# Kernel tuning notes

Measured on AMD Instinct MI355X. Metric: run time of the kernel, lower is better.

## Reference

```python
import jax, jax.numpy as jnp
import numpy as np
from jax import lax

EPS = 1e-6

def _pixel_coords(loc, H, W):
    # normalized [-1,1] xy -> continuous pixel coordinates (x in [.. W-0.5], y likewise)
    wh = jnp.array([W, H], dtype=loc.dtype)
    pos = 0.5 * (jnp.clip(loc, -1.0, 1.0) + 1.0) * wh - 0.5
    return pos[..., 0], pos[..., 1]

def token2map_agg_sparse(x, loc_orig, idx_agg, H, W):
    # scatter token features to the [H,W] map via nearest pixel of each original point,
    # normalized by per-pixel hit count (sparse-matrix formulation in the original).
    B, N, C = x.shape
    N0 = idx_agg.shape[1]
    px, py = _pixel_coords(loc_orig, H, W)
    ix = jnp.clip(jnp.round(px).astype(jnp.int32), 0, W - 1)
    iy = jnp.clip(jnp.round(py).astype(jnp.int32), 0, H - 1)
    idx_hw = (iy * W + ix + jnp.arange(B, dtype=jnp.int32)[:, None] * (H * W)).reshape(-1)
    vals = jnp.take_along_axis(x, idx_agg[..., None].astype(jnp.int32), axis=1)  # [B,N0,C]
    num = jax.ops.segment_sum(vals.reshape(B * N0, C), idx_hw, num_segments=B * H * W)
    cnt = jax.ops.segment_sum(jnp.ones((B * N0,), x.dtype), idx_hw, num_segments=B * H * W)
    fmap = num / (cnt + EPS)[:, None]
    return fmap.reshape(B, H, W, C).transpose(0, 3, 1, 2)  # NCHW

def map2token_agg_mat(fmap, loc_orig, idx_agg, agg_weight, N):
    # bilinear gather at each original point, then weighted aggregation to tokens via idx_agg
    B, C, H, W = fmap.shape
    N0 = idx_agg.shape[1]
    px, py = _pixel_coords(loc_orig, H, W)
    x0 = jnp.clip(jnp.floor(px).astype(jnp.int32), 0, W - 1)
    x1 = jnp.clip(x0 + 1, 0, W - 1)
    y0 = jnp.clip(jnp.floor(py).astype(jnp.int32), 0, H - 1)
    y1 = jnp.clip(y0 + 1, 0, H - 1)
    wx = jnp.minimum(x1.astype(px.dtype), px) - x0.astype(px.dtype)
    wy = jnp.minimum(y1.astype(py.dtype), py) - y0.astype(py.dtype)
    fm = fmap.transpose(0, 2, 3, 1).reshape(B, H * W, C)
    def gather(iy, ix):
        return jnp.take_along_axis(fm, (iy * W + ix)[..., None], axis=1)
    f = ((1 - wx) * (1 - wy))[..., None] * gather(y0, x0) \
      + (wx * (1 - wy))[..., None] * gather(y0, x1) \
      + ((1 - wx) * wy)[..., None] * gather(y1, x0) \
      + (wx * wy)[..., None] * gather(y1, x1)  # [B,N0,C]
    seg = (idx_agg.astype(jnp.int32) + jnp.arange(B, dtype=jnp.int32)[:, None] * N).reshape(-1)
    w = agg_weight.reshape(B * N0)
    wsum = jax.ops.segment_sum(w, seg, num_segments=B * N) + EPS
    wn = w / wsum[seg]
    out = jax.ops.segment_sum(f.reshape(B * N0, C) * wn[:, None], seg, num_segments=B * N)
    return out.reshape(B, N, C)

def dwconv2d(xmap, conv_w, conv_b):
    C = xmap.shape[1]
    y = lax.conv_general_dilated(xmap, conv_w, (1, 1), ((1, 1), (1, 1)),
                                 feature_group_count=C,
                                 dimension_numbers=('NCHW', 'OIHW', 'NCHW'))
    return y + conv_b[None, :, None, None]

def setup_inputs() -> dict:
    key = jax.random.key(0)
    ks = jax.random.split(key, 6)
    B, N, C, N0, H, W = 16, 1536, 768, 3072, 64, 48
    x = jax.random.normal(ks[0], (B, N, C), dtype=jnp.float32)
    loc = jax.random.uniform(ks[1], (B, N, 2), dtype=jnp.float32) * 2.0 - 1.0
    loc_orig = jax.random.uniform(ks[2], (B, N0, 2), dtype=jnp.float32) * 2.0 - 1.0
    idx_agg = jax.random.randint(ks[3], (B, N0), 0, N, dtype=jnp.int32)
    agg_weight = jax.random.uniform(ks[4], (B, N0, 1), dtype=jnp.float32)
    conv_w = jax.random.normal(ks[5], (C, 1, 3, 3), dtype=jnp.float32) * 0.1
    conv_b = jnp.zeros((C,), dtype=jnp.float32)
    return {"x": x, "loc": loc, "loc_orig": loc_orig, "idx_agg": idx_agg,
            "agg_weight": agg_weight, "H": H, "W": W,
            "conv_w": conv_w, "conv_b": conv_b}

def reference(x, loc, loc_orig, idx_agg, agg_weight, H, W, conv_w, conv_b):
    B, N, C = x.shape
    fmap = token2map_agg_sparse(x, loc_orig, idx_agg, H, W)       # [B,C,H,W]
    fmap = dwconv2d(fmap, conv_w, conv_b)                          # depthwise 3x3
    out = map2token_agg_mat(fmap, loc_orig, idx_agg, agg_weight, N)  # [B,N,C]
    return out
```

## Files before the change

kernel.cpp:

```cpp
#include <hip/hip_runtime.h>

#define B_    16
#define N_    1536
#define C_    768
#define N0_   3072
#define H_    64
#define W_    48
#define HW_   (H_ * W_)
#define NPTS  (B_ * N0_)
#define NTOK  (B_ * N_)
#define NPIX  (B_ * HW_)
#define NSCAN (NPIX + NTOK)
#define NBP   (NPIX / 256)
#define NBALL (NSCAN / 256)
#define EPS_  1e-6f
#define TY_   4
#define TX_   8
#define NTILE ((W_ / TX_) * (H_ / TY_))
#define NBCV  (B_ * NTILE)

__device__ __forceinline__ int xcd_swz(int bid, int n) {
    return (bid & 7) * (n >> 3) + (bid >> 3);
}

__global__ void k_wT(const float* __restrict__ w, float* __restrict__ wT) {
    int i = blockIdx.x * blockDim.x + threadIdx.x;
    if (i < C_ * 9) { int c = i / 9, k = i - c * 9; wT[k * C_ + c] = w[i]; }
}

__global__ void k_points(const float* __restrict__ loc_orig,
                         const int* __restrict__ idx_agg,
                         const float* __restrict__ agg_w,
                         int* __restrict__ pixkey, int4* __restrict__ ofs4,
                         float* __restrict__ wxa, float* __restrict__ wya,
                         float* __restrict__ wa,
                         int* __restrict__ cnt_pix, int* __restrict__ cnt_tok,
                         float* __restrict__ wsum) {
    int i = blockIdx.x * blockDim.x + threadIdx.x;
    if (i >= NPTS) return;
    int b = i / N0_;
    float lx = loc_orig[2 * (size_t)i];
    float ly = loc_orig[2 * (size_t)i + 1];
    lx = fminf(fmaxf(lx, -1.f), 1.f);
    ly = fminf(fmaxf(ly, -1.f), 1.f);
    float px = 0.5f * (lx + 1.f) * (float)W_ - 0.5f;
    float py = 0.5f * (ly + 1.f) * (float)H_ - 0.5f;
    int ixn = min(max((int)rintf(px), 0), W_ - 1);
    int iyn = min(max((int)rintf(py), 0), H_ - 1);
    int pk = b * HW_ + iyn * W_ + ixn;
    pixkey[i] = pk;
    int x0 = min(max((int)floorf(px), 0), W_ - 1);
    int x1 = min(x0 + 1, W_ - 1);
    int y0 = min(max((int)floorf(py), 0), H_ - 1);
    int y1 = min(y0 + 1, H_ - 1);
    wxa[i] = fminf((float)x1, px) - (float)x0;
    wya[i] = fminf((float)y1, py) - (float)y0;
    ofs4[i] = make_int4(y0 * W_ + x0, y0 * W_ + x1, y1 * W_ + x0, y1 * W_ + x1);
    float w = agg_w[i];
    wa[i] = w;
    atomicAdd(&cnt_pix[pk], 1);
    int tk = b * N_ + idx_agg[i];
    atomicAdd(&cnt_tok[tk], 1);
    atomicAdd(&wsum[tk], w);
}

__global__ __launch_bounds__(256)
void k_scanA(const int* __restrict__ cnt, int* __restrict__ pre, int* __restrict__ bsum) {
    __shared__ int sh[256];
    int b = blockIdx.x, t = threadIdx.x;
    int i = b * 256 + t;
    int v = cnt[i];
    sh[t] = v;
    __syncthreads();
    for (int d = 1; d < 256; d <<= 1) {
        int x = sh[t];
        int y = (t >= d) ? sh[t - d] : 0;
        __syncthreads();
        sh[t] = x + y;
        __syncthreads();
    }
    pre[i] = sh[t] - v;
    if (t == 255) bsum[b] = sh[255];
}

__global__ __launch_bounds__(256)
void k_scanB(const int* __restrict__ bsum, int* __restrict__ bbase,
             int* __restrict__ off_pix, int* __restrict__ off_tok) {
    __shared__ int sh[256];
    int t = threadIdx.x;
    int v = (t < NBP) ? bsum[t] : 0;
    sh[t] = v;
    __syncthreads();
    for (int d = 1; d < 256; d <<= 1) {
        int x = sh[t];
        int y = (t >= d) ? sh[t - d] : 0;
        __syncthreads();
        sh[t] = x + y;
        __syncthreads();
    }
    if (t < NBP) bbase[t] = sh[t] - v;
    __syncthreads();
    int nbt = NBALL - NBP;
    v = (t < nbt) ? bsum[NBP + t] : 0;
    sh[t] = v;
    __syncthreads();
    for (int d = 1; d < 256; d <<= 1) {
        int x = sh[t];
        int y = (t >= d) ? sh[t - d] : 0;
        __syncthreads();
        sh[t] = x + y;
        __syncthreads();
    }
    if (t < nbt) bbase[NBP + t] = sh[t] - v;
    if (t == 0) { off_pix[NPIX] = NPTS; off_tok[NTOK] = NPTS; }
}

__global__ __launch_bounds__(256)
void k_scanC(const int* __restrict__ pre, const int* __restrict__ bbase,
             int* __restrict__ off_pix, int* __restrict__ cur_pix,
             int* __restrict__ off_tok, int* __restrict__ cur_tok) {
    int b = blockIdx.x, t = threadIdx.x;
    int i = b * 256 + t;
    int val = pre[i] + bbase[b];
    if (b < NBP) { off_pix[i] = val; cur_pix[i] = val; }
    else { int j = i - NPIX; off_tok[j] = val; cur_tok[j] = val; }
}

__global__ void k_fill(const int* __restrict__ pixkey, const int* __restrict__ idx_agg,
                       const float* __restrict__ wxa, const float* __restrict__ wya,
                       const float* __restrict__ wa, const float* __restrict__ wsum,
                       int* __restrict__ cur_pix, int* __restrict__ cur_tok,
                       int* __restrict__ list_pix, int* __restrict__ list_tok,
                       float4* __restrict__ wts4) {
    int i = blockIdx.x * blockDim.x + threadIdx.x;
    if (i >= NPTS) return;
    int b = i / N0_;
    int tok = idx_agg[i];
    int tk = b * N_ + tok;
    int s1 = atomicAdd(&cur_pix[pixkey[i]], 1);
    list_pix[s1] = tk;
    int s2 = atomicAdd(&cur_tok[tk], 1);
    list_tok[s2] = i;
    float wn = wa[i] / (wsum[tk] + EPS_);
    float wx = wxa[i], wy = wya[i];
    wts4[i] = make_float4((1.f - wx) * (1.f - wy) * wn, wx * (1.f - wy) * wn,
                          (1.f - wx) * wy * wn,         wx * wy * wn);
}

template<int CC>
__global__ __launch_bounds__(CC / 4)
void k_scatter(const float4* __restrict__ x4, const int* __restrict__ off_pix,
               const int* __restrict__ list_pix, float4* __restrict__ fmap4,
               int cbase4) {
    int pk = xcd_swz(blockIdx.x, NPIX);
    int t = threadIdx.x;
    int s = off_pix[pk], e = off_pix[pk + 1];
    float4 a = make_float4(0.f, 0.f, 0.f, 0.f);
    for (int j = s; j < e; ++j) {
        int row = list_pix[j];
        float4 v = x4[(size_t)row * (C_ / 4) + cbase4 + t];
        a.x += v.x; a.y += v.y; a.z += v.z; a.w += v.w;
    }
    float sc = 1.f / ((float)(e - s) + EPS_);
    a.x *= sc; a.y *= sc; a.z *= sc; a.w *= sc;
    fmap4[(size_t)pk * (CC / 4) + t] = a;
}

template<int CC>
__global__ __launch_bounds__(CC)
void k_conv(const float* __restrict__ fmap, const float* __restrict__ wT,
            const float* __restrict__ cb, float* __restrict__ out, int cbase) {
    int logical = xcd_swz(blockIdx.x, NBCV);
    int b = logical / NTILE;
    int tile = logical % NTILE;
    int tx0 = (tile % (W_ / TX_)) * TX_;
    int ty0 = (tile / (W_ / TX_)) * TY_;
    int c = threadIdx.x;
    const float* base = fmap + (size_t)b * HW_ * CC + c;
    float v[TY_ + 2][TX_ + 2];
#pragma unroll
    for (int r = 0; r < TY_ + 2; ++r) {
        int yy = ty0 + r - 1;
        bool yok = (unsigned)yy < (unsigned)H_;
#pragma unroll
        for (int j = 0; j < TX_ + 2; ++j) {
            int xx = tx0 + j - 1;
            bool ok = yok && ((unsigned)xx < (unsigned)W_);
            v[r][j] = ok ? base[(size_t)(yy * W_ + xx) * CC] : 0.f;
        }
    }
    int cg = cbase + c;
    float k0 = wT[0 * C_ + cg], k1 = wT[1 * C_ + cg], k2 = wT[2 * C_ + cg];
    float k3 = wT[3 * C_ + cg], k4 = wT[4 * C_ + cg], k5 = wT[5 * C_ + cg];
    float k6 = wT[6 * C_ + cg], k7 = wT[7 * C_ + cg], k8 = wT[8 * C_ + cg];
    float bias = cb[cg];
    float* ob = out + (size_t)b * HW_ * CC + c;
#pragma unroll
    for (int r = 0; r < TY_; ++r) {
#pragma unroll
        for (int j = 0; j < TX_; ++j) {
            float acc = bias
                + k0 * v[r][j]     + k1 * v[r][j + 1]     + k2 * v[r][j + 2]
                + k3 * v[r + 1][j] + k4 * v[r + 1][j + 1] + k5 * v[r + 1][j + 2]
                + k6 * v[r + 2][j] + k7 * v[r + 2][j + 1] + k8 * v[r + 2][j + 2];
            ob[(size_t)((ty0 + r) * W_ + tx0 + j) * CC] = acc;
        }
    }
}

template<int CC>
__global__ __launch_bounds__(CC / 4)
void k_gather(const float4* __restrict__ conv4, const int* __restrict__ off_tok,
              const int* __restrict__ list_tok, const int4* __restrict__ ofs4,
              const float4* __restrict__ wts4, float4* __restrict__ out4,
              int cbase4) {
    int tk = xcd_swz(blockIdx.x, NTOK);
    int t = threadIdx.x;
    int b = tk / N_;
    int s = off_tok[tk], e = off_tok[tk + 1];
    const float4* bb = conv4 + (size_t)b * HW_ * (CC / 4) + t;
    float4 a = make_float4(0.f, 0.f, 0.f, 0.f);
    for (int j = s; j < e; ++j) {
        int i = list_tok[j];
        int4 o = ofs4[i];
        float4 w = wts4[i];
        float4 p0 = bb[(size_t)o.x * (CC / 4)];
        float4 p1 = bb[(size_t)o.y * (CC / 4)];
        float4 p2 = bb[(size_t)o.z * (CC / 4)];
        float4 p3 = bb[(size_t)o.w * (CC / 4)];
        a.x += w.x * p0.x + w.y * p1.x + w.z * p2.x + w.w * p3.x;
        a.y += w.x * p0.y + w.y * p1.y + w.z * p2.y + w.w * p3.y;
        a.z += w.x * p0.z + w.y * p1.z + w.z * p2.z + w.w * p3.z;
        a.w += w.x * p0.w + w.y * p1.w + w.z * p2.w + w.w * p3.w;
    }
    out4[(size_t)tk * (C_ / 4) + cbase4 + t] = a;
}

template<int CC>
static void run_chunks(const float4* x4, const int* off_pix, const int* list_pix,
                       const int* off_tok, const int* list_tok,
                       const int4* ofs4, const float4* wts4,
                       const float* wT, const float* cb,
                       float* fmap, float* convout, float* out,
                       hipStream_t stream) {
    constexpr int NCH = C_ / CC;
    for (int chunk = 0; chunk < NCH; ++chunk) {
        int cbase = chunk * CC;
        k_scatter<CC><<<NPIX, CC / 4, 0, stream>>>(
            x4, off_pix, list_pix, (float4*)fmap, cbase / 4);
        k_conv<CC><<<NBCV, CC, 0, stream>>>(fmap, wT, cb, convout, cbase);
        k_gather<CC><<<NTOK, CC / 4, 0, stream>>>(
            (const float4*)convout, off_tok, list_tok, ofs4, wts4,
            (float4*)out, cbase / 4);
    }
}

extern "C" void kernel_launch(void* const* d_in, const int* in_sizes, int n_in,
                              void* d_out, int out_size, void* d_ws, size_t ws_size,
                              hipStream_t stream) {
    const float* x        = (const float*)d_in[0];
    const float* loc_orig = (const float*)d_in[2];
    const int*   idx_agg  = (const int*)d_in[3];
    const float* agg_w    = (const float*)d_in[4];
    const float* conv_w   = (const float*)d_in[7];
    const float* conv_b   = (const float*)d_in[8];
    float* out = (float*)d_out;

    char* wsp = (char*)d_ws;
    size_t o = 0;
    auto alloc = [&](size_t bytes) -> void* {
        o = (o + 255) & ~(size_t)255;
        void* p = wsp + o;
        o += bytes;
        return p;
    };
    float*  wT       = (float*)alloc(C_ * 9 * sizeof(float));
    int*    pixkey   = (int*)alloc(NPTS * sizeof(int));
    int4*   ofs4     = (int4*)alloc(NPTS * sizeof(int4));
    float*  wxa      = (float*)alloc(NPTS * sizeof(float));
    float*  wya      = (float*)alloc(NPTS * sizeof(float));
    float*  wa       = (float*)alloc(NPTS * sizeof(float));
    float4* wts4     = (float4*)alloc(NPTS * sizeof(float4));
    int*    cnt_pix  = (int*)alloc((size_t)NSCAN * sizeof(int)
                                   + (size_t)NTOK * sizeof(float));
    int*    cnt_tok  = cnt_pix + NPIX;
    float*  wsum     = (float*)(cnt_tok + NTOK);
    int*    pre      = (int*)alloc((size_t)NSCAN * sizeof(int));
    int*    bsum     = (int*)alloc(NBALL * sizeof(int));
    int*    bbase    = (int*)alloc(NBALL * sizeof(int));
    int*    off_pix  = (int*)alloc((size_t)(NPIX + 1) * sizeof(int));
    int*    off_tok  = (int*)alloc((size_t)(NTOK + 1) * sizeof(int));
    int*    cur_pix  = (int*)alloc((size_t)NPIX * sizeof(int));
    int*    cur_tok  = (int*)alloc((size_t)NTOK * sizeof(int));
    int*    list_pix = (int*)alloc(NPTS * sizeof(int));
    int*    list_tok = (int*)alloc(NPTS * sizeof(int));

    size_t small_end = (o + 255) & ~(size_t)255;
    size_t perchan = (size_t)B_ * HW_ * 2 * sizeof(float);
    size_t avail = (ws_size > small_end + 1024) ? ws_size - small_end - 1024 : 0;
    int cc = 8;
    const int ladder[5] = {256, 128, 64, 32, 16};
    for (int k = 0; k < 5; ++k)
        if (avail >= (size_t)ladder[k] * perchan) { cc = ladder[k]; break; }

    float* fmap    = (float*)alloc((size_t)B_ * HW_ * cc * sizeof(float));
    float* convout = (float*)alloc((size_t)B_ * HW_ * cc * sizeof(float));

    hipMemsetAsync(cnt_pix, 0,
                   (size_t)NSCAN * sizeof(int) + (size_t)NTOK * sizeof(float),
                   stream);

    k_wT<<<(C_ * 9 + 255) / 256, 256, 0, stream>>>(conv_w, wT);
    k_points<<<NPTS / 256, 256, 0, stream>>>(loc_orig, idx_agg, agg_w,
                                             pixkey, ofs4, wxa, wya, wa,
                                             cnt_pix, cnt_tok, wsum);
    k_scanA<<<NBALL, 256, 0, stream>>>(cnt_pix, pre, bsum);
    k_scanB<<<1, 256, 0, stream>>>(bsum, bbase, off_pix, off_tok);
    k_scanC<<<NBALL, 256, 0, stream>>>(pre, bbase, off_pix, cur_pix, off_tok, cur_tok);
    k_fill<<<NPTS / 256, 256, 0, stream>>>(pixkey, idx_agg, wxa, wya, wa, wsum,
                                           cur_pix, cur_tok, list_pix, list_tok, wts4);

    const float4* x4 = (const float4*)x;
    switch (cc) {
        case 256: run_chunks<256>(x4, off_pix, list_pix, off_tok, list_tok, ofs4, wts4,
                                  wT, conv_b, fmap, convout, out, stream); break;
        case 128: run_chunks<128>(x4, off_pix, list_pix, off_tok, list_tok, ofs4, wts4,
                                  wT, conv_b, fmap, convout, out, stream); break;
        case  64: run_chunks< 64>(x4, off_pix, list_pix, off_tok, list_tok, ofs4, wts4,
                                  wT, conv_b, fmap, convout, out, stream); break;
        case  32: run_chunks< 32>(x4, off_pix, list_pix, off_tok, list_tok, ofs4, wts4,
                                  wT, conv_b, fmap, convout, out, stream); break;
        case  16: run_chunks< 16>(x4, off_pix, list_pix, off_tok, list_tok, ofs4, wts4,
                                  wT, conv_b, fmap, convout, out, stream); break;
        default:  run_chunks<  8>(x4, off_pix, list_pix, off_tok, list_tok, ofs4, wts4,
                                  wT, conv_b, fmap, convout, out, stream); break;
    }
}
```

Baseline: 293.3 us.

## Fuse scatter-average into depthwise conv via shared-memory halo tile

Adds a fused kernel that computes the per-pixel scatter average for each conv tile's halo directly into shared memory, then runs the 3x3 depthwise conv from LDS. This removes the intermediate fmap write and read to global memory for 256-channel chunks. In exchange it recomputes halo pixels (about 60 halo pixels per 32-pixel tile, so roughly 1.9x the scatter gathers from x). It also uses 60KB of LDS per block, which limits occupancy. The old scatter/conv path is kept as a fallback when workspace is small.

After: 316.4 us. 1.08x slower.

```diff
diff --git a/kernel.cpp b/kernel.cpp
--- a/kernel.cpp
+++ b/kernel.cpp
@@ -16,6 +16,9 @@
 #define EPS_  1e-6f
 #define TY_   4
 #define TX_   8
+#define HTY_  (TY_ + 2)
+#define HTX_  (TX_ + 2)
+#define NHALO (HTY_ * HTX_)
 #define NTILE ((W_ / TX_) * (H_ / TY_))
 #define NBCV  (B_ * NTILE)
 
@@ -148,47 +151,51 @@
 }
 
 template<int CC>
-__global__ __launch_bounds__(CC / 4)
-void k_scatter(const float4* __restrict__ x4, const int* __restrict__ off_pix,
-               const int* __restrict__ list_pix, float4* __restrict__ fmap4,
-               int cbase4) {
-    int pk = xcd_swz(blockIdx.x, NPIX);
-    int t = threadIdx.x;
-    int s = off_pix[pk], e = off_pix[pk + 1];
-    float4 a = make_float4(0.f, 0.f, 0.f, 0.f);
-    for (int j = s; j < e; ++j) {
-        int row = list_pix[j];
-        float4 v = x4[(size_t)row * (C_ / 4) + cbase4 + t];
-        a.x += v.x; a.y += v.y; a.z += v.z; a.w += v.w;
-    }
-    float sc = 1.f / ((float)(e - s) + EPS_);
-    a.x *= sc; a.y *= sc; a.z *= sc; a.w *= sc;
-    fmap4[(size_t)pk * (CC / 4) + t] = a;
-}
-
-template<int CC>
-__global__ __launch_bounds__(CC)
-void k_conv(const float* __restrict__ fmap, const float* __restrict__ wT,
-            const float* __restrict__ cb, float* __restrict__ out, int cbase) {
+__global__ __launch_bounds__(512, 4)
+void k_sconv(const float4* __restrict__ x4, const int* __restrict__ off_pix,
+             const int* __restrict__ list_pix, const float* __restrict__ wT,
+             const float* __restrict__ cb, float* __restrict__ out, int cbase) {
+    __shared__ float4 sh4[NHALO * (CC / 4)];
     int logical = xcd_swz(blockIdx.x, NBCV);
     int b = logical / NTILE;
     int tile = logical % NTILE;
     int tx0 = (tile % (W_ / TX_)) * TX_;
     int ty0 = (tile / (W_ / TX_)) * TY_;
-    int c = threadIdx.x;
-    const float* base = fmap + (size_t)b * HW_ * CC + c;
-    float v[TY_ + 2][TX_ + 2];
-#pragma unroll
-    for (int r = 0; r < TY_ + 2; ++r) {
-        int yy = ty0 + r - 1;
-        bool yok = (unsigned)yy < (unsigned)H_;
-#pragma unroll
-        for (int j = 0; j < TX_ + 2; ++j) {
-            int xx = tx0 + j - 1;
-            bool ok = yok && ((unsigned)xx < (unsigned)W_);
-            v[r][j] = ok ? base[(size_t)(yy * W_ + xx) * CC] : 0.f;
-        }
-    }
+    {
+        int slot = threadIdx.x >> 6;
+        int t = threadIdx.x & 63;
+#pragma unroll
+        for (int it = 0; it < (NHALO + 7) / 8; ++it) {
+            int hp = it * 8 + slot;
+            if (hp < NHALO) {
+                int hy = hp / HTX_, hx = hp - hy * HTX_;
+                int yy = ty0 + hy - 1, xx = tx0 + hx - 1;
+                float4 a = make_float4(0.f, 0.f, 0.f, 0.f);
+                if ((unsigned)yy < (unsigned)H_ && (unsigned)xx < (unsigned)W_) {
+                    int pk = b * HW_ + yy * W_ + xx;
+                    int s = off_pix[pk], e = off_pix[pk + 1];
+                    for (int j = s; j < e; ++j) {
+                        int row = list_pix[j];
+                        float4 v = x4[(size_t)row * (C_ / 4) + (cbase >> 2) + t];
+                        a.x += v.x; a.y += v.y; a.z += v.z; a.w += v.w;
+                    }
+                    float sc = 1.f / ((float)(e - s) + EPS_);
+                    a.x *= sc; a.y *= sc; a.z *= sc; a.w *= sc;
+                }
+                sh4[hp * (CC / 4) + t] = a;
+            }
+        }
+    }
+    __syncthreads();
+    int c = threadIdx.x & (CC - 1);
+    int half = threadIdx.x >> 8;
+    const float* sh = (const float*)sh4;
+    float v[TY_ / 2 + 2][HTX_];
+#pragma unroll
+    for (int r = 0; r < TY_ / 2 + 2; ++r)
+#pragma unroll
+        for (int j = 0; j < HTX_; ++j)
+            v[r][j] = sh[((half * 2 + r) * HTX_ + j) * CC + c];
     int cg = cbase + c;
     float k0 = wT[0 * C_ + cg], k1 = wT[1 * C_ + cg], k2 = wT[2 * C_ + cg];
     float k3 = wT[3 * C_ + cg], k4 = wT[4 * C_ + cg], k5 = wT[5 * C_ + cg];
@@ -196,14 +203,14 @@
     float bias = cb[cg];
     float* ob = out + (size_t)b * HW_ * CC + c;
 #pragma unroll
-    for (int r = 0; r < TY_; ++r) {
+    for (int r = 0; r < TY_ / 2; ++r) {
 #pragma unroll
         for (int j = 0; j < TX_; ++j) {
             float acc = bias
                 + k0 * v[r][j]     + k1 * v[r][j + 1]     + k2 * v[r][j + 2]
                 + k3 * v[r + 1][j] + k4 * v[r + 1][j + 1] + k5 * v[r + 1][j + 2]
                 + k6 * v[r + 2][j] + k7 * v[r + 2][j + 1] + k8 * v[r + 2][j + 2];
-            ob[(size_t)((ty0 + r) * W_ + tx0 + j) * CC] = acc;
+            ob[(size_t)((ty0 + half * 2 + r) * W_ + tx0 + j) * CC] = acc;
         }
     }
 }
@@ -237,6 +244,67 @@
 }
 
 template<int CC>
+__global__ __launch_bounds__(CC / 4)
+void k_scat_s(const float4* __restrict__ x4, const int* __restrict__ off_pix,
+              const int* __restrict__ list_pix, float4* __restrict__ fmap4,
+              int cbase4) {
+    int pk = xcd_swz(blockIdx.x, NPIX);
+    int t = threadIdx.x;
+    int s = off_pix[pk], e = off_pix[pk + 1];
+    float4 a = make_float4(0.f, 0.f, 0.f, 0.f);
+    for (int j = s; j < e; ++j) {
+        int row = list_pix[j];
+        float4 v = x4[(size_t)row * (C_ / 4) + cbase4 + t];
+        a.x += v.x; a.y += v.y; a.z += v.z; a.w += v.w;
+    }
+    float sc = 1.f / ((float)(e - s) + EPS_);
+    a.x *= sc; a.y *= sc; a.z *= sc; a.w *= sc;
+    fmap4[(size_t)pk * (CC / 4) + t] = a;
+}
+
+template<int CC>
+__global__ __launch_bounds__(CC)
+void k_conv_s(const float* __restrict__ fmap, const float* __restrict__ wT,
+              const float* __restrict__ cb, float* __restrict__ out, int cbase) {
+    int logical = xcd_swz(blockIdx.x, NBCV);
+    int b = logical / NTILE;
+    int tile = logical % NTILE;
+    int tx0 = (tile % (W_ / TX_)) * TX_;
+    int ty0 = (tile / (W_ / TX_)) * TY_;
+    int c = threadIdx.x;
+    const float* base = fmap + (size_t)b * HW_ * CC + c;
+    float v[TY_ + 2][TX_ + 2];
+#pragma unroll
+    for (int r = 0; r < TY_ + 2; ++r) {
+        int yy = ty0 + r - 1;
+        bool yok = (unsigned)yy < (unsigned)H_;
+#pragma unroll
+        for (int j = 0; j < TX_ + 2; ++j) {
+            int xx = tx0 + j - 1;
+            bool ok = yok && ((unsigned)xx < (unsigned)W_);
+            v[r][j] = ok ? base[(size_t)(yy * W_ + xx) * CC] : 0.f;
+        }
+    }
+    int cg = cbase + c;
+    float k0 = wT[0 * C_ + cg], k1 = wT[1 * C_ + cg], k2 = wT[2 * C_ + cg];
+    float k3 = wT[3 * C_ + cg], k4 = wT[4 * C_ + cg], k5 = wT[5 * C_ + cg];
+    float k6 = wT[6 * C_ + cg], k7 = wT[7 * C_ + cg], k8 = wT[8 * C_ + cg];
+    float bias = cb[cg];
+    float* ob = out + (size_t)b * HW_ * CC + c;
+#pragma unroll
+    for (int r = 0; r < TY_; ++r) {
+#pragma unroll
+        for (int j = 0; j < TX_; ++j) {
+            float acc = bias
+                + k0 * v[r][j]     + k1 * v[r][j + 1]     + k2 * v[r][j + 2]
+                + k3 * v[r + 1][j] + k4 * v[r + 1][j + 1] + k5 * v[r + 1][j + 2]
+                + k6 * v[r + 2][j] + k7 * v[r + 2][j + 1] + k8 * v[r + 2][j + 2];
+            ob[(size_t)((ty0 + r) * W_ + tx0 + j) * CC] = acc;
+        }
+    }
+}
+
+template<int CC>
 static void run_chunks(const float4* x4, const int* off_pix, const int* list_pix,
                        const int* off_tok, const int* list_tok,
                        const int4* ofs4, const float4* wts4,
@@ -246,9 +314,9 @@
     constexpr int NCH = C_ / CC;
     for (int chunk = 0; chunk < NCH; ++chunk) {
         int cbase = chunk * CC;
-        k_scatter<CC><<<NPIX, CC / 4, 0, stream>>>(
+        k_scat_s<CC><<<NPIX, CC / 4, 0, stream>>>(
             x4, off_pix, list_pix, (float4*)fmap, cbase / 4);
-        k_conv<CC><<<NBCV, CC, 0, stream>>>(fmap, wT, cb, convout, cbase);
+        k_conv_s<CC><<<NBCV, CC, 0, stream>>>(fmap, wT, cb, convout, cbase);
         k_gather<CC><<<NTOK, CC / 4, 0, stream>>>(
             (const float4*)convout, off_tok, list_tok, ofs4, wts4,
             (float4*)out, cbase / 4);
@@ -296,20 +364,12 @@
     int*    list_tok = (int*)alloc(NPTS * sizeof(int));
 
     size_t small_end = (o + 255) & ~(size_t)255;
-    size_t perchan = (size_t)B_ * HW_ * 2 * sizeof(float);
+    size_t slab = (size_t)B_ * HW_ * 256 * sizeof(float);
     size_t avail = (ws_size > small_end + 1024) ? ws_size - small_end - 1024 : 0;
-    int cc = 8;
-    const int ladder[5] = {256, 128, 64, 32, 16};
-    for (int k = 0; k < 5; ++k)
-        if (avail >= (size_t)ladder[k] * perchan) { cc = ladder[k]; break; }
-
-    float* fmap    = (float*)alloc((size_t)B_ * HW_ * cc * sizeof(float));
-    float* convout = (float*)alloc((size_t)B_ * HW_ * cc * sizeof(float));
 
     hipMemsetAsync(cnt_pix, 0,
                    (size_t)NSCAN * sizeof(int) + (size_t)NTOK * sizeof(float),
                    stream);
-
     k_wT<<<(C_ * 9 + 255) / 256, 256, 0, stream>>>(conv_w, wT);
     k_points<<<NPTS / 256, 256, 0, stream>>>(loc_orig, idx_agg, agg_w,
                                              pixkey, ofs4, wxa, wya, wa,
@@ -321,18 +381,44 @@
                                            cur_pix, cur_tok, list_pix, list_tok, wts4);
 
     const float4* x4 = (const float4*)x;
-    switch (cc) {
-        case 256: run_chunks<256>(x4, off_pix, list_pix, off_tok, list_tok, ofs4, wts4,
-                                  wT, conv_b, fmap, convout, out, stream); break;
-        case 128: run_chunks<128>(x4, off_pix, list_pix, off_tok, list_tok, ofs4, wts4,
-                                  wT, conv_b, fmap, convout, out, stream); break;
-        case  64: run_chunks< 64>(x4, off_pix, list_pix, off_tok, list_tok, ofs4, wts4,
-                                  wT, conv_b, fmap, convout, out, stream); break;
-        case  32: run_chunks< 32>(x4, off_pix, list_pix, off_tok, list_tok, ofs4, wts4,
-                                  wT, conv_b, fmap, convout, out, stream); break;
-        case  16: run_chunks< 16>(x4, off_pix, list_pix, off_tok, list_tok, ofs4, wts4,
-                                  wT, conv_b, fmap, convout, out, stream); break;
-        default:  run_chunks<  8>(x4, off_pix, list_pix, off_tok, list_tok, ofs4, wts4,
-                                  wT, conv_b, fmap, convout, out, stream); break;
-    }
-}
+
+    if (avail >= slab) {
+        float* convout = (float*)alloc(slab);
+        for (int chunk = 0; chunk < 3; ++chunk) {
+            int cbase = chunk * 256;
+            k_sconv<256><<<NBCV, 512, 0, stream>>>(
+                x4, off_pix, list_pix, wT, conv_b, convout, cbase);
+            k_gather<256><<<NTOK, 64, 0, stream>>>(
+                (const float4*)convout, off_tok, list_tok, ofs4, wts4,
+                (float4*)out, cbase / 4);
+        }
+    } else {
+        size_t perchan = (size_t)B_ * HW_ * 2 * sizeof(float);
+        int cc = 8;
+        const int ladder[5] = {256, 128, 64, 32, 16};
+        for (int k = 0; k < 5; ++k)
+            if (avail >= (size_t)ladder[k] * perchan) { cc = ladder[k]; break; }
+        float* fmap    = (float*)alloc((size_t)B_ * HW_ * cc * sizeof(float));
+        float* convout = (float*)alloc((size_t)B_ * HW_ * cc * sizeof(float));
+        switch (cc) {
+            case 256: run_chunks<256>(x4, off_pix, list_pix, off_tok, list_tok,
+                                      ofs4, wts4, wT, conv_b, fmap, convout, out,
+                                      stream); break;
+            case 128: run_chunks<128>(x4, off_pix, list_pix, off_tok, list_tok,
+                                      ofs4, wts4, wT, conv_b, fmap, convout, out,
+                                      stream); break;
+            case  64: run_chunks< 64>(x4, off_pix, list_pix, off_tok, list_tok,
+                                      ofs4, wts4, wT, conv_b, fmap, convout, out,
+                                      stream); break;
+            case  32: run_chunks< 32>(x4, off_pix, list_pix, off_tok, list_tok,
+                                      ofs4, wts4, wT, conv_b, fmap, convout, out,
+                                      stream); break;
+            case  16: run_chunks< 16>(x4, off_pix, list_pix, off_tok, list_tok,
+                                      ofs4, wts4, wT, conv_b, fmap, convout, out,
+                                      stream); break;
+            default:  run_chunks<  8>(x4, off_pix, list_pix, off_tok, list_tok,
+                                      ofs4, wts4, wT, conv_b, fmap, convout, out,
+                                      stream); break;
+        }
+    }
+}
```
